# Performance work log

Hardware: AMD Instinct MI355X
Metric: run time of the kernel (lower is better)

The kernel has to match this reference:

```python
import jax, jax.numpy as jnp
import numpy as np

NUM_BINS = 30
MIN_BW = 0.001
MIN_BH = 0.001
MIN_D = 0.001
LI, UI = 0.0, 1.0   # input bounds
LO, UO = 0.0, 1.0   # output bounds
DERIV_OUT = (UO - LO) / (UI - LI)
EPS = 1e-6


def _cumparams(unnorm, lower, upper, min_size):
    # softmax -> min-size floor -> cumsum -> pad zero -> affine to [lower, upper]
    p = jax.nn.softmax(unnorm, axis=-1)
    p = min_size + (1.0 - min_size * NUM_BINS) * p
    cp = jnp.cumsum(p, axis=-1)
    cp = jnp.pad(cp, [(0, 0), (1, 0)])            # [V, nb+1], starts at 0
    cp = (upper - lower) * cp + lower
    return cp, cp[..., 1:] - cp[..., :-1]         # cum, bin sizes


def _spline_forward(inputs, uw, uh, ud):
    V = uw.shape[0]
    cw, widths = _cumparams(uw, LI, UI, MIN_BW)   # [V, nb+1], [V, nb]
    ch, heights = _cumparams(uh, LO, UO, MIN_BH)

    # boundary derivative constant: softplus(c) = 1 - MIN_D  =>  deriv = 1 at edges
    c = np.log(np.exp(1.0 - MIN_D) - 1.0).astype(np.float32)
    edge = jnp.full((V, 1), c, dtype=uw.dtype)
    derivs = MIN_D + jax.nn.softplus(jnp.concatenate([edge, ud, edge], axis=-1))  # [V, nb+1]

    delta = heights / widths                      # [V, nb]
    cb = cw.at[..., -1].add(EPS)                  # bin-search boundaries

    below = inputs < LI
    above = inputs > UI
    inside = ~(below | above)
    x = jnp.clip(inputs, LI, UI)                  # safe values for masked-out points

    # per-point bin search: [B, V, nb+1] comparison then sum
    bin_idx = jnp.sum(x[..., None] >= cb[None], axis=-1) - 1
    bin_idx = jnp.clip(bin_idx, 0, NUM_BINS - 1)  # [B, V] int

    v = jnp.arange(V)[None, :]
    icw = cw[v, bin_idx]
    ibw = widths[v, bin_idx]
    ich = ch[v, bin_idx]
    idl = delta[v, bin_idx]
    d0 = derivs[v, bin_idx]
    d1 = derivs[v, bin_idx + 1]
    ih = heights[v, bin_idx]

    theta = (x - icw) / ibw
    t1mt = theta * (1.0 - theta)
    den = idl + (d0 + d1 - 2.0 * idl) * t1mt
    out_in = ich + ih * (idl * theta * theta + d0 * t1mt) / den
    numd = (idl * idl) * (d1 * theta * theta + 2.0 * idl * t1mt + d0 * (1.0 - theta) ** 2)
    lad_in = jnp.log(numd) - 2.0 * jnp.log(den)

    out = jnp.where(below, LO + (inputs - LI) * DERIV_OUT,
          jnp.where(above, UO + (inputs - UI) * DERIV_OUT, out_in))
    lad = jnp.where(inside, lad_in, 0.0)
    return out, lad


def setup_inputs() -> dict:
    key = jax.random.key(0)
    k1, k2, k3, k4 = jax.random.split(key, 4)
    B, V = 16384, 512
    inputs = jax.random.uniform(k1, (B, V), dtype=jnp.float32)
    uw = 0.3 * jax.random.normal(k2, (V, NUM_BINS), dtype=jnp.float32)
    uh = 0.3 * jax.random.normal(k3, (V, NUM_BINS), dtype=jnp.float32)
    ud = 0.5405 + 0.1 * jax.random.normal(k4, (V, NUM_BINS - 1), dtype=jnp.float32)
    return {"inputs": inputs, "unnormalized_widths": uw,
            "unnormalized_heights": uh, "unnormalized_derivatives": ud}


def reference(inputs, unnormalized_widths, unnormalized_heights, unnormalized_derivatives):
    return _spline_forward(inputs, unnormalized_widths, unnormalized_heights,
                           unnormalized_derivatives)
```

## Files before the change

kernel.cpp:

```cpp
#include <hip/hip_runtime.h>
#include <math.h>

#define NB 30
#define PKG 96
#define PKS 99
#define VMAX 512

__device__ float g_pk[VMAX * PKG];

__device__ __forceinline__ float softplus_safe(float x) {
    return fmaxf(x, 0.0f) + log1pf(__expf(-fabsf(x)));
}

__device__ __forceinline__ void cum_from_unnorm(const float* __restrict__ u,
                                                int v, float min_size,
                                                float* __restrict__ dst ) {
    float r[NB];
#pragma unroll
    for (int k = 0; k < NB; ++k) r[k] = u[v * NB + k];
    float m = r[0];
#pragma unroll
    for (int k = 1; k < NB; ++k) m = fmaxf(m, r[k]);
    float e[NB];
    float s = 0.f;
#pragma unroll
    for (int k = 0; k < NB; ++k) { e[k] = __expf(r[k] - m); s += e[k]; }
    const float fac = (1.0f - min_size * (float)NB) / s;
    float run = 0.f;
    dst[0] = 0.0f;
#pragma unroll
    for (int k = 0; k < NB; ++k) {
        run += min_size + fac * e[k];
        dst[k + 1] = run;
    }
}

__global__ void rqs_params_kernel(const float* __restrict__ uw,
                                  const float* __restrict__ uh,
                                  const float* __restrict__ ud, int V) {
    int v = blockIdx.x * 64 + threadIdx.x;
    if (v >= V) return;
    float cw[NB + 1], ch[NB + 1], dv[NB + 1];
    cum_from_unnorm(uw, v, 0.001f, cw);
    cum_from_unnorm(uh, v, 0.001f, ch);
    dv[0] = 1.0f;
    dv[NB] = 1.0f;
#pragma unroll
    for (int k = 1; k < NB; ++k)
        dv[k] = 0.001f + softplus_safe(ud[v * (NB - 1) + k - 1]);

    float* d = &g_pk[v * PKG];
#pragma unroll
    for (int k = 0; k <= NB; ++k) {
        d[3 * k + 0] = cw[k];
        d[3 * k + 1] = ch[k];
        d[3 * k + 2] = dv[k];
    }
    d[93] = 3.0e38f;
    d[94] = 0.0f;
    d[95] = 0.0f;
}

__global__ __launch_bounds__(256) void rqs_main_kernel(
        const float* __restrict__ x_in, float* __restrict__ out,
        float* __restrict__ lad, int B, int V, int nct, int rowTiles) {
    __shared__ float pkS[64 * PKS];

    const int tid = threadIdx.x;
    const int colTile = blockIdx.x % nct;
    const int rowBlk  = blockIdx.x / nct;
    const int colbase = colTile * 64;

    for (int i = tid; i < 64 * (PKG / 4); i += 256) {
        const int c = i / (PKG / 4);
        const int q = i - c * (PKG / 4);
        const float4 val = *(const float4*)&g_pk[(size_t)(colbase + c) * PKG + q * 4];
        float* dst = &pkS[c * PKS + q * 4];
        dst[0] = val.x; dst[1] = val.y; dst[2] = val.z; dst[3] = val.w;
    }
    __syncthreads();

    const int c = tid & 63;
    const int w = tid >> 6;
    const int col = colbase + c;
    const float* __restrict__ pc = &pkS[c * PKS];

    const int rowStride = rowTiles * 16;

    for (int base = rowBlk * 16; base < B; base += rowStride) {
        const int r0 = base + w * 4;

        float xv[4], xc[4];
        int jj[4];
#pragma unroll
        for (int u = 0; u < 4; ++u) {
            const int row = r0 + u;
            xv[u] = (row < B) ? x_in[(size_t)row * V + col] : 0.5f;
            xc[u] = fminf(fmaxf(xv[u], 0.0f), 1.0f);
        }

#pragma unroll
        for (int u = 0; u < 4; ++u) jj[u] = (pc[48] <= xc[u]) ? 48 : 0;
#pragma unroll
        for (int u = 0; u < 4; ++u) jj[u] += (pc[jj[u] + 24] <= xc[u]) ? 24 : 0;
#pragma unroll
        for (int u = 0; u < 4; ++u) jj[u] += (pc[jj[u] + 12] <= xc[u]) ? 12 : 0;
#pragma unroll
        for (int u = 0; u < 4; ++u) jj[u] += (pc[jj[u] +  6] <= xc[u]) ?  6 : 0;
#pragma unroll
        for (int u = 0; u < 4; ++u) jj[u] += (pc[jj[u] +  3] <= xc[u]) ?  3 : 0;
#pragma unroll
        for (int u = 0; u < 4; ++u) jj[u] = min(jj[u], 3 * (NB - 1));

        float cwl[4], chl[4], d0[4], cwr[4], chr[4], d1[4];
#pragma unroll
        for (int u = 0; u < 4; ++u) {
            const float* p = pc + jj[u];
            cwl[u] = p[0]; chl[u] = p[1]; d0[u] = p[2];
            cwr[u] = p[3]; chr[u] = p[4]; d1[u] = p[5];
        }

#pragma unroll
        for (int u = 0; u < 4; ++u) {
            const int row = r0 + u;
            if (row >= B) continue;
            const float wd = cwr[u] - cwl[u];
            const float h  = chr[u] - chl[u];
            const float winv = __builtin_amdgcn_rcpf(wd);
            const float delta = h * winv;
            const float theta = (xc[u] - cwl[u]) * winv;
            const float omt = 1.0f - theta;
            const float t1mt = theta * omt;
            const float th2 = theta * theta;
            const float den = delta + (d0[u] + d1[u] - 2.0f * delta) * t1mt;
            const float dinv = __builtin_amdgcn_rcpf(den);
            const float out_in = chl[u] + h * (delta * th2 + d0[u] * t1mt) * dinv;
            const float dd = delta * delta;
            const float numd = dd * (d1[u] * th2 + 2.0f * delta * t1mt + d0[u] * omt * omt);
            const float lad_in = __logf(numd * dinv * dinv);

            const bool inside = (xv[u] >= 0.0f) && (xv[u] <= 1.0f);
            out[(size_t)row * V + col] = inside ? out_in : xv[u];
            lad[(size_t)row * V + col] = inside ? lad_in : 0.0f;
        }
    }
}

extern "C" void kernel_launch(void* const* d_in, const int* in_sizes, int n_in,
                              void* d_out, int out_size, void* d_ws, size_t ws_size,
                              hipStream_t stream) {
    const float* x  = (const float*)d_in[0];
    const float* uw = (const float*)d_in[1];
    const float* uh = (const float*)d_in[2];
    const float* ud = (const float*)d_in[3];

    const int V = in_sizes[1] / NB;
    const int B = in_sizes[0] / V;

    float* out = (float*)d_out;
    float* lad = out + (size_t)B * V;

    rqs_params_kernel<<<(V + 63) / 64, 64, 0, stream>>>(uw, uh, ud, V);

    const int nct = V / 64;
    const int rowTiles = 192;
    rqs_main_kernel<<<nct * rowTiles, 256, 0, stream>>>(x, out, lad, B, V, nct, rowTiles);
}
```

Baseline: 38.52 us.

## Fuse spline parameter setup into main kernel and deepen per-thread row batching

Drops the separate parameter kernel and its global scratch buffer. Each block now computes softmax, cumsum and softplus for its 64 columns straight into shared memory, saving a launch and a global round trip. The first three binary-search levels use knot values cached in registers. Each thread handles 8 rows per pass with nontemporal loads, and a specialised V=512 template drops the bounds checks. The cost is that every block recomputes the parameters serially on 64 threads.

```diff
diff --git a/kernel.cpp b/kernel.cpp
--- a/kernel.cpp
+++ b/kernel.cpp
@@ -2,146 +2,146 @@
 #include <math.h>
 
 #define NB 30
-#define PKG 96
-#define PKS 99
-#define VMAX 512
+#define PS 99
+#define TPB 256
 
-__device__ float g_pk[VMAX * PKG];
-
-__device__ __forceinline__ float softplus_safe(float x) {
+__device__ __forceinline__ float softplus_f(float x) {
     return fmaxf(x, 0.0f) + log1pf(__expf(-fabsf(x)));
 }
 
-__device__ __forceinline__ void cum_from_unnorm(const float* __restrict__ u,
-                                                int v, float min_size,
-                                                float* __restrict__ dst ) {
+__device__ __forceinline__ void stage_cum(const float* __restrict__ u, int v,
+                                          float* __restrict__ dst) {
     float r[NB];
 #pragma unroll
     for (int k = 0; k < NB; ++k) r[k] = u[v * NB + k];
     float m = r[0];
 #pragma unroll
     for (int k = 1; k < NB; ++k) m = fmaxf(m, r[k]);
-    float e[NB];
     float s = 0.f;
 #pragma unroll
-    for (int k = 0; k < NB; ++k) { e[k] = __expf(r[k] - m); s += e[k]; }
-    const float fac = (1.0f - min_size * (float)NB) / s;
+    for (int k = 0; k < NB; ++k) s += __expf(r[k] - m);
+    const float fac = (1.0f - 0.001f * (float)NB) / s;
     float run = 0.f;
-    dst[0] = 0.0f;
+    dst[0] = 0.f;
 #pragma unroll
     for (int k = 0; k < NB; ++k) {
-        run += min_size + fac * e[k];
-        dst[k + 1] = run;
+        run += 0.001f + fac * __expf(r[k] - m);
+        dst[3 * (k + 1)] = run;
     }
 }
 
-__global__ void rqs_params_kernel(const float* __restrict__ uw,
-                                  const float* __restrict__ uh,
-                                  const float* __restrict__ ud, int V) {
-    int v = blockIdx.x * 64 + threadIdx.x;
-    if (v >= V) return;
-    float cw[NB + 1], ch[NB + 1], dv[NB + 1];
-    cum_from_unnorm(uw, v, 0.001f, cw);
-    cum_from_unnorm(uh, v, 0.001f, ch);
-    dv[0] = 1.0f;
-    dv[NB] = 1.0f;
-#pragma unroll
-    for (int k = 1; k < NB; ++k)
-        dv[k] = 0.001f + softplus_safe(ud[v * (NB - 1) + k - 1]);
+template <int VC, bool EXACT>
+__global__ __launch_bounds__(TPB, 4) void rqs_fused_kernel(
+        const float* __restrict__ x_in,
+        const float* __restrict__ uw,
+        const float* __restrict__ uh,
+        const float* __restrict__ ud,
+        float* __restrict__ out,
+        float* __restrict__ lad,
+        int B, int Vrt, int nct, int rowTiles) {
+    const int V = VC ? VC : Vrt;
 
-    float* d = &g_pk[v * PKG];
-#pragma unroll
-    for (int k = 0; k <= NB; ++k) {
-        d[3 * k + 0] = cw[k];
-        d[3 * k + 1] = ch[k];
-        d[3 * k + 2] = dv[k];
-    }
-    d[93] = 3.0e38f;
-    d[94] = 0.0f;
-    d[95] = 0.0f;
-}
-
-__global__ __launch_bounds__(256) void rqs_main_kernel(
-        const float* __restrict__ x_in, float* __restrict__ out,
-        float* __restrict__ lad, int B, int V, int nct, int rowTiles) {
-    __shared__ float pkS[64 * PKS];
+    __shared__ float pkS[64 * PS];
 
     const int tid = threadIdx.x;
     const int colTile = blockIdx.x % nct;
     const int rowBlk  = blockIdx.x / nct;
     const int colbase = colTile * 64;
 
-    for (int i = tid; i < 64 * (PKG / 4); i += 256) {
-        const int c = i / (PKG / 4);
-        const int q = i - c * (PKG / 4);
-        const float4 val = *(const float4*)&g_pk[(size_t)(colbase + c) * PKG + q * 4];
-        float* dst = &pkS[c * PKS + q * 4];
-        dst[0] = val.x; dst[1] = val.y; dst[2] = val.z; dst[3] = val.w;
+    if (tid < 64) {
+        const int v = colbase + tid;
+        float* pcw = &pkS[tid * PS];
+        stage_cum(uw, v, pcw);
+        stage_cum(uh, v, pcw + 1);
+        pcw[2] = 1.0f;
+        pcw[3 * NB + 2] = 1.0f;
+#pragma unroll
+        for (int k = 1; k < NB; ++k)
+            pcw[3 * k + 2] = 0.001f + softplus_f(ud[v * (NB - 1) + k - 1]);
+        pcw[93] = 3.0e38f;
     }
     __syncthreads();
 
     const int c = tid & 63;
     const int w = tid >> 6;
     const int col = colbase + c;
-    const float* __restrict__ pc = &pkS[c * PKS];
+    const float* __restrict__ pc = &pkS[c * PS];
 
-    const int rowStride = rowTiles * 16;
+    const float c12 = pc[12], c24 = pc[24], c36 = pc[36], c48 = pc[48];
+    const float c60 = pc[60], c72 = pc[72], c84 = pc[84];
 
-    for (int base = rowBlk * 16; base < B; base += rowStride) {
-        const int r0 = base + w * 4;
+    const int passRows = 32;
 
-        float xv[4], xc[4];
-        int jj[4];
+    for (int base = rowBlk * passRows; base < B; base += rowTiles * passRows) {
+        const int r0 = base + w * 8;
+
+        float xv[8], xc[8];
+        int jj[8];
 #pragma unroll
-        for (int u = 0; u < 4; ++u) {
+        for (int u = 0; u < 8; ++u) {
             const int row = r0 + u;
-            xv[u] = (row < B) ? x_in[(size_t)row * V + col] : 0.5f;
-            xc[u] = fminf(fmaxf(xv[u], 0.0f), 1.0f);
+            const bool ok = EXACT || (row < B);
+            xv[u] = ok ? __builtin_nontemporal_load(&x_in[(size_t)row * V + col]) : 0.5f;
         }
+#pragma unroll
+        for (int u = 0; u < 8; ++u) xc[u] = fminf(fmaxf(xv[u], 0.0f), 1.0f);
 
 #pragma unroll
-        for (int u = 0; u < 4; ++u) jj[u] = (pc[48] <= xc[u]) ? 48 : 0;
+        for (int u = 0; u < 8; ++u) {
+            const float xq = xc[u];
+            const bool b1 = (c48 <= xq);
+            const float l2 = b1 ? c72 : c24;
+            const bool b2 = (l2 <= xq);
+            const float t0 = b2 ? c36 : c12;
+            const float t1 = b2 ? c84 : c60;
+            const float l3 = b1 ? t1 : t0;
+            const bool b3 = (l3 <= xq);
+            jj[u] = (b1 ? 48 : 0) + (b2 ? 24 : 0) + (b3 ? 12 : 0);
+        }
 #pragma unroll
-        for (int u = 0; u < 4; ++u) jj[u] += (pc[jj[u] + 24] <= xc[u]) ? 24 : 0;
+        for (int u = 0; u < 8; ++u) jj[u] += (pc[jj[u] + 6] <= xc[u]) ? 6 : 0;
 #pragma unroll
-        for (int u = 0; u < 4; ++u) jj[u] += (pc[jj[u] + 12] <= xc[u]) ? 12 : 0;
+        for (int u = 0; u < 8; ++u) jj[u] += (pc[jj[u] + 3] <= xc[u]) ? 3 : 0;
 #pragma unroll
-        for (int u = 0; u < 4; ++u) jj[u] += (pc[jj[u] +  6] <= xc[u]) ?  6 : 0;
-#pragma unroll
-        for (int u = 0; u < 4; ++u) jj[u] += (pc[jj[u] +  3] <= xc[u]) ?  3 : 0;
-#pragma unroll
-        for (int u = 0; u < 4; ++u) jj[u] = min(jj[u], 3 * (NB - 1));
-
-        float cwl[4], chl[4], d0[4], cwr[4], chr[4], d1[4];
-#pragma unroll
-        for (int u = 0; u < 4; ++u) {
-            const float* p = pc + jj[u];
-            cwl[u] = p[0]; chl[u] = p[1]; d0[u] = p[2];
-            cwr[u] = p[3]; chr[u] = p[4]; d1[u] = p[5];
-        }
+        for (int u = 0; u < 8; ++u) jj[u] = min(jj[u], 3 * (NB - 1));
 
 #pragma unroll
-        for (int u = 0; u < 4; ++u) {
-            const int row = r0 + u;
-            if (row >= B) continue;
-            const float wd = cwr[u] - cwl[u];
-            const float h  = chr[u] - chl[u];
-            const float winv = __builtin_amdgcn_rcpf(wd);
-            const float delta = h * winv;
-            const float theta = (xc[u] - cwl[u]) * winv;
-            const float omt = 1.0f - theta;
-            const float t1mt = theta * omt;
-            const float th2 = theta * theta;
-            const float den = delta + (d0[u] + d1[u] - 2.0f * delta) * t1mt;
-            const float dinv = __builtin_amdgcn_rcpf(den);
-            const float out_in = chl[u] + h * (delta * th2 + d0[u] * t1mt) * dinv;
-            const float dd = delta * delta;
-            const float numd = dd * (d1[u] * th2 + 2.0f * delta * t1mt + d0[u] * omt * omt);
-            const float lad_in = __logf(numd * dinv * dinv);
+        for (int g = 0; g < 2; ++g) {
+            float cwl[4], cwr[4], chl[4], chr[4], d0[4], d1[4];
+#pragma unroll
+            for (int q = 0; q < 4; ++q) {
+                const float* p = pc + jj[g * 4 + q];
+                cwl[q] = p[0]; cwr[q] = p[3];
+                chl[q] = p[1]; chr[q] = p[4];
+                d0[q]  = p[2]; d1[q]  = p[5];
+            }
+#pragma unroll
+            for (int q = 0; q < 4; ++q) {
+                const int u = g * 4 + q;
+                const int row = r0 + u;
+                const bool ok = EXACT || (row < B);
+                const float wd = cwr[q] - cwl[q];
+                const float h  = chr[q] - chl[q];
+                const float winv = __builtin_amdgcn_rcpf(wd);
+                const float delta = h * winv;
+                const float theta = (xc[u] - cwl[q]) * winv;
+                const float omt = 1.0f - theta;
+                const float t1mt = theta * omt;
+                const float th2 = theta * theta;
+                const float den = delta + (d0[q] + d1[q] - 2.0f * delta) * t1mt;
+                const float dinv = __builtin_amdgcn_rcpf(den);
+                const float out_in = chl[q] + h * (delta * th2 + d0[q] * t1mt) * dinv;
+                const float numd = delta * delta *
+                    (d1[q] * th2 + 2.0f * delta * t1mt + d0[q] * omt * omt);
+                const float lad_in = __logf(numd * dinv * dinv);
 
-            const bool inside = (xv[u] >= 0.0f) && (xv[u] <= 1.0f);
-            out[(size_t)row * V + col] = inside ? out_in : xv[u];
-            lad[(size_t)row * V + col] = inside ? lad_in : 0.0f;
+                const bool inside = (xv[u] >= 0.0f) && (xv[u] <= 1.0f);
+                if (ok) {
+                    const size_t idx = (size_t)row * V + col;
+                    out[idx] = inside ? out_in : xv[u];
+                    lad[idx] = inside ? lad_in : 0.0f;
+                }
+            }
         }
     }
 }
@@ -160,9 +160,16 @@
     float* out = (float*)d_out;
     float* lad = out + (size_t)B * V;
 
-    rqs_params_kernel<<<(V + 63) / 64, 64, 0, stream>>>(uw, uh, ud, V);
-
-    const int nct = V / 64;
-    const int rowTiles = 192;
-    rqs_main_kernel<<<nct * rowTiles, 256, 0, stream>>>(x, out, lad, B, V, nct, rowTiles);
+    if (V == 512 && (B % 32) == 0) {
+        const int nct = 512 / 64;
+        const int rowTiles = (B / 32 + 3) / 4 >= 128 ? 128 : (B / 32);
+        rqs_fused_kernel<512, true><<<nct * rowTiles, TPB, 0, stream>>>(
+            x, uw, uh, ud, out, lad, B, V, nct, rowTiles);
+    } else {
+        const int nct = V / 64;
+        int rowTiles = (B + 31) / 32;
+        if (rowTiles > 128) rowTiles = 128;
+        rqs_fused_kernel<0, false><<<nct * rowTiles, TPB, 0, stream>>>(
+            x, uw, uh, ud, out, lad, B, V, nct, rowTiles);
+    }
 }
```

Result: faster. 35.34 us (-8.3%).
